# Kernel tuning notes

Measured on AMD Instinct MI355X. Metric: run time of the kernel, lower is better.

Reference implementation:

```python
import jax, jax.numpy as jnp
import numpy as np

N, M, G = 50000, 400000, 128   # nodes, undirected edges, graphs
FN, FE, L, O = 128, 32, 128, 128
MAX_LV = 3


def setup_inputs() -> dict:
    rng = np.random.default_rng(0)
    key = jax.random.key(0)
    ks = jax.random.split(key, 12)
    # random multigraph without self-loops; directed edges interleaved so that
    # edge 2i = (u->v) and edge 2i+1 = (v->u) (reverse edge = e ^ 1)
    u = rng.integers(0, N, size=M)
    v = (u + 1 + rng.integers(0, N - 1, size=M)) % N
    src = np.empty(2 * M, dtype=np.int32)
    dst = np.empty(2 * M, dtype=np.int32)
    src[0::2], src[1::2] = u, v
    dst[0::2], dst[1::2] = v, u
    graph_ids = np.sort(rng.integers(0, G, size=N)).astype(np.int32)

    def lin(k, fan_in, fan_out):
        return jax.random.normal(k, (fan_in, fan_out), jnp.float32) / np.sqrt(fan_in)

    return {
        "node_feat": jax.random.normal(ks[0], (N, FN), jnp.float32),
        "edge_feat": jax.random.normal(ks[1], (2 * M, FE), jnp.float32),
        "w_n2l_W": lin(ks[2], FN, L), "w_n2l_b": jnp.zeros((L,), jnp.float32),
        "w_e2l_W": lin(ks[3], FE, L), "w_e2l_b": jnp.zeros((L,), jnp.float32),
        "conv_W": lin(ks[4], L, L),   "conv_b": jnp.zeros((L,), jnp.float32),
        "out_W": lin(ks[5], L, O),    "out_b": jnp.zeros((O,), jnp.float32),
        "edge_src": jnp.asarray(src),
        "edge_dst": jnp.asarray(dst),
        "graph_ids": jnp.asarray(graph_ids),
        "num_graphs": G,
    }


def _swap_reverse(msgs):
    # message of the reverse directed edge: pairs are interleaved (2i, 2i+1)
    E, D = msgs.shape
    return msgs.reshape(E // 2, 2, D)[:, ::-1, :].reshape(E, D)


def reference(node_feat, edge_feat, w_n2l_W, w_n2l_b, w_e2l_W, w_e2l_b,
              conv_W, conv_b, out_W, out_b, edge_src, edge_dst, graph_ids,
              num_graphs):
    n_nodes = node_feat.shape[0]
    # n2e_sp @ (W_n node_feat): gather source-node linear features onto edges
    input_node_linear = node_feat @ w_n2l_W + w_n2l_b          # [N, L]
    input_message = input_node_linear[edge_src]                # [E, L]
    input_message = input_message + (edge_feat @ w_e2l_W + w_e2l_b)
    cur = jax.nn.relu(input_message)                           # input_potential
    for _ in range(MAX_LV):
        # e2e_sp @ cur: sum of messages into src node, minus reverse edge
        node_agg = jax.ops.segment_sum(cur, edge_dst, num_segments=n_nodes)
        e2epool = node_agg[edge_src] - _swap_reverse(cur)      # [E, L]
        cur = jax.nn.relu(e2epool @ conv_W + conv_b + input_message)
    # e2n_sp @ cur: sum edge messages into destination nodes
    e2npool = jax.ops.segment_sum(cur, edge_dst, num_segments=n_nodes)
    hidden_msg = jax.nn.relu(e2npool)                          # [N, L]
    reluact = jax.nn.relu(hidden_msg @ out_W + out_b)          # [N, O]
    # subg_sp @ reluact: pool nodes per graph
    y = jax.ops.segment_sum(reluact, graph_ids, num_segments=num_graphs)
    return jax.nn.relu(y)                                      # [G, O]
```

## Files before the change

kernel.cpp:

```cpp
#include <hip/hip_runtime.h>
#include <hip/hip_bf16.h>
#include <stdint.h>

typedef __attribute__((ext_vector_type(8))) short short8;
typedef __attribute__((ext_vector_type(4))) float f32x4;

#if defined(__has_builtin)
#if __has_builtin(__builtin_amdgcn_cvt_pk_bf16_f32)
#define HAVE_PK_BF16 1
#endif
#endif

__device__ __forceinline__ float b2f(ushort u) {
  union { uint32_t i; float f; } v; v.i = ((uint32_t)u) << 16; return v.f;
}
__device__ __forceinline__ ushort f2b_sw(float f) {
  union { float f; uint32_t i; } v; v.f = f;
  uint32_t x = v.i;
  uint32_t r = x + 0x7FFFu + ((x >> 16) & 1u);
  return (ushort)(r >> 16);
}
__device__ __forceinline__ uint pk2(float lo, float hi) {
#ifdef HAVE_PK_BF16
  auto r = __builtin_amdgcn_cvt_pk_bf16_f32(lo, hi);
  union { decltype(r) v; uint u; } c; c.v = r; return c.u;
#else
  return (uint)f2b_sw(lo) | ((uint)f2b_sw(hi) << 16);
#endif
}
__device__ __forceinline__ ushort f2b(float f) {
#ifdef HAVE_PK_BF16
  return (ushort)(pk2(f, 0.f) & 0xFFFFu);
#else
  return f2b_sw(f);
#endif
}
__device__ __forceinline__ float lo2f(uint v) { return b2f((ushort)(v & 0xFFFFu)); }
__device__ __forceinline__ float hi2f(uint v) { return b2f((ushort)(v >> 16)); }

__device__ __forceinline__ uint4 pkf8(float4 a, float4 b) {
  uint4 o;
  o.x = pk2(a.x, a.y); o.y = pk2(a.z, a.w);
  o.z = pk2(b.x, b.y); o.w = pk2(b.z, b.w);
  return o;
}
__device__ __forceinline__ uint sub2(uint a, uint b) {
  return pk2(lo2f(a) - lo2f(b), hi2f(a) - hi2f(b));
}
__device__ __forceinline__ uint4 sub8(uint4 a, uint4 b) {
  uint4 o; o.x = sub2(a.x,b.x); o.y = sub2(a.y,b.y); o.z = sub2(a.z,b.z); o.w = sub2(a.w,b.w); return o;
}
__device__ __forceinline__ uint addrelu2(uint a, uint b) {
  return pk2(fmaxf(lo2f(a) + lo2f(b), 0.f), fmaxf(hi2f(a) + hi2f(b), 0.f));
}
__device__ __forceinline__ uint4 addrelu8(uint4 a, uint4 b) {
  uint4 o; o.x = addrelu2(a.x,b.x); o.y = addrelu2(a.y,b.y);
  o.z = addrelu2(a.z,b.z); o.w = addrelu2(a.w,b.w); return o;
}
__device__ __forceinline__ uint relu2(uint v) {
  uint lo = (v & 0x8000u) ? 0u : (v & 0xFFFFu);
  uint hi = (v & 0x80000000u) ? 0u : (v & 0xFFFF0000u);
  return lo | hi;
}
__device__ __forceinline__ uint4 relu8(uint4 v) {
  uint4 o; o.x = relu2(v.x); o.y = relu2(v.y); o.z = relu2(v.z); o.w = relu2(v.w); return o;
}

__global__ void zero_ints(int* __restrict__ p, int n) {
  int i = blockIdx.x * blockDim.x + threadIdx.x;
  if (i < n) p[i] = 0;
}

__global__ void prep_weights(const float* __restrict__ wn, const float* __restrict__ we,
                             const float* __restrict__ cw, const float* __restrict__ ow,
                             const float* __restrict__ cb, const float* __restrict__ be,
                             ushort* __restrict__ wnT, ushort* __restrict__ weT,
                             ushort* __restrict__ cweT, ushort* __restrict__ owT,
                             float* __restrict__ cbe) {
  int i = blockIdx.x * blockDim.x + threadIdx.x;
  if (i < 16384) {
    int n = i >> 7, k = i & 127; wnT[n*128+k] = f2b(wn[k*128+n]);
  } else if (i < 32768) {
    int j = i - 16384; int n = j >> 7, k = j & 127; owT[n*128+k] = f2b(ow[k*128+n]);
  } else if (i < 53248) {
    int j = i - 32768;
    int n = j / 160, k = j % 160;
    cweT[n*160+k] = (k < 128) ? f2b(cw[k*128+n]) : f2b(we[(k-128)*128+n]);
  } else if (i < 57344) {
    int j = i - 53248; int n = j >> 5, k = j & 31; weT[n*32+k] = f2b(we[k*128+n]);
  } else if (i < 57472) {
    int j = i - 57344; cbe[j] = cb[j] + be[j];
  }
}

__global__ void count_dst(const int* __restrict__ dst, int* __restrict__ counts, int E) {
  for (int i = blockIdx.x * blockDim.x + threadIdx.x; i < E; i += gridDim.x * blockDim.x)
    atomicAdd(&counts[dst[i]], 1);
}
__global__ __launch_bounds__(1024) void scan_offsets(
    const int* __restrict__ counts, int* __restrict__ off,
    int* __restrict__ cursor, int N) {
  __shared__ int part[1024];
  int t = threadIdx.x;
  int chunk = (N + 1023) >> 10;
  int lo = t * chunk, hi = min(lo + chunk, N);
  int s = 0;
  for (int i = lo; i < hi; ++i) s += counts[i];
  part[t] = s;
  __syncthreads();
  for (int d = 1; d < 1024; d <<= 1) {
    int v = (t >= d) ? part[t - d] : 0;
    __syncthreads();
    part[t] += v;
    __syncthreads();
  }
  int run = (t > 0) ? part[t - 1] : 0;
  for (int i = lo; i < hi; ++i) {
    off[i] = run; cursor[i] = run; run += counts[i];
  }
  if (t == 1023) off[N] = part[1023];
}
__global__ void fill_csr(const int* __restrict__ dst, int* __restrict__ cursor,
                         int* __restrict__ eids, int E) {
  for (int i = blockIdx.x * blockDim.x + threadIdx.x; i < E; i += gridDim.x * blockDim.x) {
    int p = atomicAdd(&cursor[dst[i]], 1);
    eids[p] = i;
  }
}

__global__ __launch_bounds__(256) void node_linear(
    const float* __restrict__ nf, const ushort* __restrict__ wnT,
    const float* __restrict__ bn, ushort* __restrict__ inl, int N) {
  __shared__ ushort Als[64][136];
  __shared__ ushort Bls[128][136];
  int tid = threadIdx.x;
  int n0 = blockIdx.x * 64;
  {
    int row = tid >> 1, h = tid & 1;
    const uint4* gp = (const uint4*)(wnT + row*128 + h*64);
    uint4* lp = (uint4*)&Bls[row][h*64];
    #pragma unroll
    for (int i = 0; i < 8; ++i) lp[i] = gp[i];
  }
  {
    int r = tid >> 2, q = tid & 3;
    int n = n0 + r;
    uint4* lp = (uint4*)&Als[r][q*32];
    if (n < N) {
      const float4* fp = (const float4*)(nf + (size_t)n*128 + q*32);
      #pragma unroll
      for (int i = 0; i < 4; ++i) lp[i] = pkf8(fp[2*i], fp[2*i+1]);
    } else {
      uint4 z = {0,0,0,0};
      #pragma unroll
      for (int i = 0; i < 4; ++i) lp[i] = z;
    }
  }
  __syncthreads();
  int l = tid & 63, w = tid >> 6, quad = l >> 4, mr = l & 15;
  f32x4 acc[8];
  #pragma unroll
  for (int nt = 0; nt < 8; ++nt) acc[nt] = (f32x4){0.f,0.f,0.f,0.f};
  #pragma unroll
  for (int kk = 0; kk < 4; ++kk) {
    short8 a = *(const short8*)&Als[w*16 + mr][kk*32 + quad*8];
    #pragma unroll
    for (int nt = 0; nt < 8; ++nt) {
      short8 b = *(const short8*)&Bls[nt*16 + mr][kk*32 + quad*8];
      acc[nt] = __builtin_amdgcn_mfma_f32_16x16x32_bf16(a, b, acc[nt], 0, 0, 0);
    }
  }
  #pragma unroll
  for (int nt = 0; nt < 8; ++nt) {
    int col = nt*16 + mr;
    float bias = bn[col];
    #pragma unroll
    for (int rg = 0; rg < 4; ++rg) {
      int n = n0 + w*16 + quad*4 + rg;
      if (n < N) inl[(size_t)n*128 + col] = f2b(acc[nt][rg] + bias);
    }
  }
}

__global__ __launch_bounds__(256) void edge_init(
    const float* __restrict__ ef, const ushort* __restrict__ weT,
    const float* __restrict__ be, const int* __restrict__ esrc,
    const ushort* __restrict__ inl, ushort* __restrict__ cur,
    ushort* __restrict__ efb, int E) {
  __shared__ ushort Als[64][40];
  __shared__ ushort Cls[64][136];
  int tid = threadIdx.x;
  int e0 = blockIdx.x * 64;
  int l = tid & 63, w = tid >> 6, quad = l >> 4, mr = l & 15;
  int r = tid >> 2, q = tid & 3;

  short8 bfrag[2];
  #pragma unroll
  for (int nt = 0; nt < 2; ++nt)
    bfrag[nt] = *(const short8*)(weT + (size_t)(w*32 + nt*16 + mr)*32 + quad*8);

  {
    const float4* fp = (const float4*)(ef + (size_t)(e0 + r)*32 + q*8);
    uint4 pk = pkf8(fp[0], fp[1]);
    *(uint4*)&Als[r][q*8] = pk;
    if (efb) *(uint4*)(efb + (size_t)(e0 + r)*32 + q*8) = pk;
  }
  __syncthreads();

  int col0 = w*32 + mr, col1 = w*32 + 16 + mr;
  float bias0 = be[col0], bias1 = be[col1];
  #pragma unroll
  for (int m = 0; m < 4; ++m) {
    short8 a = *(const short8*)&Als[m*16 + mr][quad*8];
    f32x4 zero = (f32x4){0.f,0.f,0.f,0.f};
    f32x4 acc0 = __builtin_amdgcn_mfma_f32_16x16x32_bf16(a, bfrag[0], zero, 0, 0, 0);
    f32x4 acc1 = __builtin_amdgcn_mfma_f32_16x16x32_bf16(a, bfrag[1], zero, 0, 0, 0);
    #pragma unroll
    for (int rg = 0; rg < 4; ++rg) {
      int row = m*16 + quad*4 + rg;
      Cls[row][col0] = f2b(acc0[rg] + bias0);
      Cls[row][col1] = f2b(acc1[rg] + bias1);
    }
  }
  __syncthreads();

  {
    int e = e0 + r;
    int s = esrc[e];
    const uint4* cl = (const uint4*)&Cls[r][q*32];
    const uint4* ip = (const uint4*)(inl + (size_t)s*128 + q*32);
    uint4* op = (uint4*)(cur + (size_t)e*128 + q*32);
    #pragma unroll
    for (int i = 0; i < 4; ++i) op[i] = addrelu8(cl[i], ip[i]);
  }
}

__global__ __launch_bounds__(256) void segsum(
    const ushort* __restrict__ cur, const int* __restrict__ off,
    const int* __restrict__ eids, ushort* __restrict__ nagg, int N) {
  int w = threadIdx.x >> 6, l = threadIdx.x & 63;
  int n = blockIdx.x * 4 + w;
  if (n >= N) return;
  int i = off[n], end = off[n + 1];
  float s0 = 0.f, s1 = 0.f;
  for (; i + 8 <= end; i += 8) {
    int e[8]; uint v[8];
    #pragma unroll
    for (int j = 0; j < 8; ++j) e[j] = eids[i + j];
    #pragma unroll
    for (int j = 0; j < 8; ++j) v[j] = *(const uint*)(cur + (size_t)e[j]*128 + 2*l);
    #pragma unroll
    for (int j = 0; j < 8; ++j) { s0 += lo2f(v[j]); s1 += hi2f(v[j]); }
  }
  for (; i < end; ++i) {
    int ea = eids[i];
    uint va = *(const uint*)(cur + (size_t)ea*128 + 2*l);
    s0 += lo2f(va); s1 += hi2f(va);
  }
  *(uint*)(nagg + (size_t)n*128 + 2*l) = pk2(s0, s1);
}

__global__ __launch_bounds__(256) void conv_step(
    ushort* __restrict__ cur, const ushort* __restrict__ nagg,
    const ushort* __restrict__ inl, const ushort* __restrict__ efb,
    const float* __restrict__ ef, const ushort* __restrict__ cweT,
    const float* __restrict__ cbe, const int* __restrict__ esrc, int E) {
  __shared__ ushort Als[64][168];
  int tid = threadIdx.x;
  int e0 = blockIdx.x * 64;
  int l = tid & 63, w = tid >> 6, quad = l >> 4, mr = l & 15;
  int r = tid >> 2, q = tid & 3;

  short8 bfrag[2][5];
  #pragma unroll
  for (int nt = 0; nt < 2; ++nt) {
    const ushort* bp = cweT + (size_t)(w*32 + nt*16 + mr) * 160;
    #pragma unroll
    for (int kk = 0; kk < 5; ++kk)
      bfrag[nt][kk] = *(const short8*)(bp + kk*32 + quad*8);
  }

  {
    int e = e0 + r;
    int s = esrc[e];
    const uint4* cp = (const uint4*)(cur + (size_t)(e ^ 1)*128 + q*32);
    const uint4* np = (const uint4*)(nagg + (size_t)s*128 + q*32);
    uint4* lp = (uint4*)&Als[r][q*32];
    #pragma unroll
    for (int i = 0; i < 4; ++i) lp[i] = sub8(np[i], cp[i]);
    if (efb) {
      *(uint4*)&Als[r][128 + q*8] = *(const uint4*)(efb + (size_t)e*32 + q*8);
    } else {
      const float4* fp = (const float4*)(ef + (size_t)e*32 + q*8);
      *(uint4*)&Als[r][128 + q*8] = pkf8(fp[0], fp[1]);
    }
  }
  __syncthreads();

  int col0 = w*32 + mr, col1 = w*32 + 16 + mr;
  float bias0 = cbe[col0], bias1 = cbe[col1];
  f32x4 acc0[4], acc1[4];
  #pragma unroll
  for (int m = 0; m < 4; ++m) {
    acc0[m] = (f32x4){0.f,0.f,0.f,0.f};
    acc1[m] = (f32x4){0.f,0.f,0.f,0.f};
    #pragma unroll
    for (int kk = 0; kk < 5; ++kk) {
      short8 a = *(const short8*)&Als[m*16 + mr][kk*32 + quad*8];
      acc0[m] = __builtin_amdgcn_mfma_f32_16x16x32_bf16(a, bfrag[0][kk], acc0[m], 0, 0, 0);
      acc1[m] = __builtin_amdgcn_mfma_f32_16x16x32_bf16(a, bfrag[1][kk], acc1[m], 0, 0, 0);
    }
  }
  __syncthreads();

  #pragma unroll
  for (int m = 0; m < 4; ++m) {
    #pragma unroll
    for (int rg = 0; rg < 4; ++rg) {
      int row = m*16 + quad*4 + rg;
      Als[row][col0] = f2b(acc0[m][rg] + bias0);
      Als[row][col1] = f2b(acc1[m][rg] + bias1);
    }
  }
  __syncthreads();

  {
    int e = e0 + r;
    int s = esrc[e];
    const uint4* cl = (const uint4*)&Als[r][q*32];
    const uint4* ip = (const uint4*)(inl + (size_t)s*128 + q*32);
    uint4* op = (uint4*)(cur + (size_t)e*128 + q*32);
    #pragma unroll
    for (int i = 0; i < 4; ++i) op[i] = addrelu8(cl[i], ip[i]);
  }
}

__global__ __launch_bounds__(256) void out_linear(
    const ushort* __restrict__ nagg, const ushort* __restrict__ owT,
    const float* __restrict__ ob, ushort* __restrict__ ract, int N) {
  __shared__ ushort Als[64][136];
  __shared__ ushort Bls[128][136];
  int tid = threadIdx.x;
  int n0 = blockIdx.x * 64;
  {
    int row = tid >> 1, h = tid & 1;
    const uint4* gp = (const uint4*)(owT + row*128 + h*64);
    uint4* lp = (uint4*)&Bls[row][h*64];
    #pragma unroll
    for (int i = 0; i < 8; ++i) lp[i] = gp[i];
  }
  {
    int r = tid >> 2, q = tid & 3;
    int n = n0 + r;
    uint4* lp = (uint4*)&Als[r][q*32];
    if (n < N) {
      const uint4* gp = (const uint4*)(nagg + (size_t)n*128 + q*32);
      #pragma unroll
      for (int i = 0; i < 4; ++i) lp[i] = relu8(gp[i]);
    } else {
      uint4 z = {0,0,0,0};
      #pragma unroll
      for (int i = 0; i < 4; ++i) lp[i] = z;
    }
  }
  __syncthreads();
  int l = tid & 63, w = tid >> 6, quad = l >> 4, mr = l & 15;
  f32x4 acc[8];
  #pragma unroll
  for (int nt = 0; nt < 8; ++nt) acc[nt] = (f32x4){0.f,0.f,0.f,0.f};
  #pragma unroll
  for (int kk = 0; kk < 4; ++kk) {
    short8 a = *(const short8*)&Als[w*16 + mr][kk*32 + quad*8];
    #pragma unroll
    for (int nt = 0; nt < 8; ++nt) {
      short8 b = *(const short8*)&Bls[nt*16 + mr][kk*32 + quad*8];
      acc[nt] = __builtin_amdgcn_mfma_f32_16x16x32_bf16(a, b, acc[nt], 0, 0, 0);
    }
  }
  #pragma unroll
  for (int nt = 0; nt < 8; ++nt) {
    int col = nt*16 + mr;
    float bias = ob[col];
    #pragma unroll
    for (int rg = 0; rg < 4; ++rg) {
      int n = n0 + w*16 + quad*4 + rg;
      if (n < N) ract[(size_t)n*128 + col] = f2b(fmaxf(acc[nt][rg] + bias, 0.f));
    }
  }
}

__global__ void graph_offsets(const int* __restrict__ gids, int* __restrict__ goff,
                              int N, int G) {
  int i = blockIdx.x * blockDim.x + threadIdx.x;
  if (i > N) return;
  int pg = (i == 0) ? -1 : gids[i - 1];
  int cg = (i == N) ? G : gids[i];
  for (int g = pg + 1; g <= cg; ++g) goff[g] = i;
}

__global__ __launch_bounds__(256) void graph_pool(
    const ushort* __restrict__ ract, const int* __restrict__ goff,
    float* __restrict__ out, int G) {
  __shared__ float red0[256];
  __shared__ float red1[256];
  int g = blockIdx.x;
  int t = threadIdx.x;
  int c2 = t & 63, rp = t >> 6;
  int beg = goff[g], end = goff[g + 1];
  float s0 = 0.f, s1 = 0.f;
  for (int n = beg + rp; n < end; n += 4) {
    uint v = *(const uint*)(ract + (size_t)n*128 + 2*c2);
    s0 += lo2f(v); s1 += hi2f(v);
  }
  red0[t] = s0; red1[t] = s1;
  __syncthreads();
  if (rp == 0) {
    float v0 = red0[c2] + red0[c2 + 64] + red0[c2 + 128] + red0[c2 + 192];
    float v1 = red1[c2] + red1[c2 + 64] + red1[c2 + 128] + red1[c2 + 192];
    float2 o; o.x = fmaxf(v0, 0.f); o.y = fmaxf(v1, 0.f);
    *(float2*)(out + (size_t)g*128 + 2*c2) = o;
  }
}

extern "C" void kernel_launch(void* const* d_in, const int* in_sizes, int n_in,
                              void* d_out, int out_size, void* d_ws, size_t ws_size,
                              hipStream_t stream) {
  const float* node_feat = (const float*)d_in[0];
  const float* edge_feat = (const float*)d_in[1];
  const float* wn = (const float*)d_in[2];
  const float* bn = (const float*)d_in[3];
  const float* we = (const float*)d_in[4];
  const float* be = (const float*)d_in[5];
  const float* cw = (const float*)d_in[6];
  const float* cb = (const float*)d_in[7];
  const float* ow = (const float*)d_in[8];
  const float* ob = (const float*)d_in[9];
  const int* esrc = (const int*)d_in[10];
  const int* edst = (const int*)d_in[11];
  const int* gids = (const int*)d_in[12];
  int N = in_sizes[0] / 128;
  int E = in_sizes[10];
  int G = out_size / 128;
  float* out = (float*)d_out;

  char* p = (char*)d_ws;
  auto alloc = [&](size_t bytes) {
    char* r = p;
    p += (bytes + 255) & ~(size_t)255;
    return r;
  };
  ushort* cur     = (ushort*)alloc((size_t)E * 128 * 2);
  ushort* inl     = (ushort*)alloc((size_t)N * 128 * 2);
  ushort* nagg    = (ushort*)alloc((size_t)N * 128 * 2);
  int*    eids    = (int*)   alloc((size_t)E * 4);
  int*    counts  = (int*)   alloc((size_t)N * 4);
  int*    off     = (int*)   alloc((size_t)(N + 1) * 4);
  int*    cursor  = (int*)   alloc((size_t)N * 4);
  int*    goff    = (int*)   alloc((size_t)(G + 1) * 4);
  ushort* wnT     = (ushort*)alloc(128 * 128 * 2);
  ushort* weT     = (ushort*)alloc(128 * 32 * 2);
  ushort* cweT    = (ushort*)alloc(128 * 160 * 2);
  ushort* owT     = (ushort*)alloc(128 * 128 * 2);
  float*  cbe     = (float*) alloc(128 * 4);
  ushort* efb     = (ushort*)alloc((size_t)E * 32 * 2);
  if ((size_t)(p - (char*)d_ws) > ws_size) efb = nullptr;
  ushort* ract    = inl;
  (void)n_in;

  zero_ints<<<(N + 255) / 256, 256, 0, stream>>>(counts, N);
  prep_weights<<<225, 256, 0, stream>>>(wn, we, cw, ow, cb, be, wnT, weT, cweT, owT, cbe);
  count_dst<<<1024, 256, 0, stream>>>(edst, counts, E);
  scan_offsets<<<1, 1024, 0, stream>>>(counts, off, cursor, N);
  fill_csr<<<1024, 256, 0, stream>>>(edst, cursor, eids, E);

  node_linear<<<(N + 63) / 64, 256, 0, stream>>>(node_feat, wnT, bn, inl, N);
  edge_init<<<E / 64, 256, 0, stream>>>(edge_feat, weT, be, esrc, inl, cur, efb, E);

  for (int it = 0; it < 3; ++it) {
    segsum<<<(N + 3) / 4, 256, 0, stream>>>(cur, off, eids, nagg, N);
    conv_step<<<E / 64, 256, 0, stream>>>(cur, nagg, inl, efb, edge_feat, cweT, cbe, esrc, E);
  }
  segsum<<<(N + 3) / 4, 256, 0, stream>>>(cur, off, eids, nagg, N);
  out_linear<<<(N + 63) / 64, 256, 0, stream>>>(nagg, owT, ob, ract, N);
  graph_offsets<<<(N + 256) / 256, 256, 0, stream>>>(gids, goff, N, G);
  graph_pool<<<G, 256, 0, stream>>>(ract, goff, out, G);
}
```

Baseline: 1.188 ms.

## Interleave node aggregate and input-linear rows, widen segsum gathers across half-waves

```diff
diff --git a/kernel.cpp b/kernel.cpp
--- a/kernel.cpp
+++ b/kernel.cpp
@@ -130,7 +130,7 @@
 
 __global__ __launch_bounds__(256) void node_linear(
     const float* __restrict__ nf, const ushort* __restrict__ wnT,
-    const float* __restrict__ bn, ushort* __restrict__ inl, int N) {
+    const float* __restrict__ bn, ushort* __restrict__ ni, int N) {
   __shared__ ushort Als[64][136];
   __shared__ ushort Bls[128][136];
   int tid = threadIdx.x;
@@ -177,7 +177,7 @@
     #pragma unroll
     for (int rg = 0; rg < 4; ++rg) {
       int n = n0 + w*16 + quad*4 + rg;
-      if (n < N) inl[(size_t)n*128 + col] = f2b(acc[nt][rg] + bias);
+      if (n < N) ni[(size_t)n*256 + 128 + col] = f2b(acc[nt][rg] + bias);
     }
   }
 }
@@ -185,7 +185,7 @@
 __global__ __launch_bounds__(256) void edge_init(
     const float* __restrict__ ef, const ushort* __restrict__ weT,
     const float* __restrict__ be, const int* __restrict__ esrc,
-    const ushort* __restrict__ inl, ushort* __restrict__ cur,
+    const ushort* __restrict__ ni, ushort* __restrict__ cur,
     ushort* __restrict__ efb, int E) {
   __shared__ ushort Als[64][40];
   __shared__ ushort Cls[64][136];
@@ -199,11 +199,19 @@
   for (int nt = 0; nt < 2; ++nt)
     bfrag[nt] = *(const short8*)(weT + (size_t)(w*32 + nt*16 + mr)*32 + quad*8);
 
-  {
-    const float4* fp = (const float4*)(ef + (size_t)(e0 + r)*32 + q*8);
+  int e = e0 + r;
+  int s = esrc[e];
+  {
+    const float4* fp = (const float4*)(ef + (size_t)e*32 + q*8);
     uint4 pk = pkf8(fp[0], fp[1]);
     *(uint4*)&Als[r][q*8] = pk;
-    if (efb) *(uint4*)(efb + (size_t)(e0 + r)*32 + q*8) = pk;
+    if (efb) *(uint4*)(efb + (size_t)e*32 + q*8) = pk;
+  }
+  uint4 irow[4];
+  {
+    const uint4* ip = (const uint4*)(ni + (size_t)s*256 + 128 + q*32);
+    #pragma unroll
+    for (int i = 0; i < 4; ++i) irow[i] = ip[i];
   }
   __syncthreads();
 
@@ -225,46 +233,60 @@
   __syncthreads();
 
   {
-    int e = e0 + r;
-    int s = esrc[e];
     const uint4* cl = (const uint4*)&Cls[r][q*32];
-    const uint4* ip = (const uint4*)(inl + (size_t)s*128 + q*32);
     uint4* op = (uint4*)(cur + (size_t)e*128 + q*32);
     #pragma unroll
-    for (int i = 0; i < 4; ++i) op[i] = addrelu8(cl[i], ip[i]);
+    for (int i = 0; i < 4; ++i) op[i] = addrelu8(cl[i], irow[i]);
   }
 }
 
 __global__ __launch_bounds__(256) void segsum(
     const ushort* __restrict__ cur, const int* __restrict__ off,
-    const int* __restrict__ eids, ushort* __restrict__ nagg, int N) {
+    const int* __restrict__ eids, ushort* __restrict__ ni, int N) {
   int w = threadIdx.x >> 6, l = threadIdx.x & 63;
   int n = blockIdx.x * 4 + w;
   if (n >= N) return;
-  int i = off[n], end = off[n + 1];
-  float s0 = 0.f, s1 = 0.f;
-  for (; i + 8 <= end; i += 8) {
-    int e[8]; uint v[8];
-    #pragma unroll
-    for (int j = 0; j < 8; ++j) e[j] = eids[i + j];
-    #pragma unroll
-    for (int j = 0; j < 8; ++j) v[j] = *(const uint*)(cur + (size_t)e[j]*128 + 2*l);
-    #pragma unroll
-    for (int j = 0; j < 8; ++j) { s0 += lo2f(v[j]); s1 += hi2f(v[j]); }
-  }
-  for (; i < end; ++i) {
-    int ea = eids[i];
-    uint va = *(const uint*)(cur + (size_t)ea*128 + 2*l);
-    s0 += lo2f(va); s1 += hi2f(va);
-  }
-  *(uint*)(nagg + (size_t)n*128 + 2*l) = pk2(s0, s1);
+  int c8 = l & 31;
+  int half = l >> 5;
+  int beg = off[n], end = off[n + 1];
+  float s0 = 0.f, s1 = 0.f, s2 = 0.f, s3 = 0.f;
+  int i = beg;
+  for (; i + 16 <= end; i += 16) {
+    uint2 v[8];
+    #pragma unroll
+    for (int j = 0; j < 8; ++j) {
+      int e = eids[i + 2*j + half];
+      v[j] = *(const uint2*)(cur + (size_t)e*128 + c8*4);
+    }
+    #pragma unroll
+    for (int j = 0; j < 8; ++j) {
+      s0 += lo2f(v[j].x); s1 += hi2f(v[j].x);
+      s2 += lo2f(v[j].y); s3 += hi2f(v[j].y);
+    }
+  }
+  for (; i + 2 <= end; i += 2) {
+    int e = eids[i + half];
+    uint2 v = *(const uint2*)(cur + (size_t)e*128 + c8*4);
+    s0 += lo2f(v.x); s1 += hi2f(v.x); s2 += lo2f(v.y); s3 += hi2f(v.y);
+  }
+  if (i < end && half == 0) {
+    int e = eids[i];
+    uint2 v = *(const uint2*)(cur + (size_t)e*128 + c8*4);
+    s0 += lo2f(v.x); s1 += hi2f(v.x); s2 += lo2f(v.y); s3 += hi2f(v.y);
+  }
+  s0 += __shfl_xor(s0, 32); s1 += __shfl_xor(s1, 32);
+  s2 += __shfl_xor(s2, 32); s3 += __shfl_xor(s3, 32);
+  if (half == 0) {
+    uint2 o; o.x = pk2(s0, s1); o.y = pk2(s2, s3);
+    *(uint2*)(ni + (size_t)n*256 + c8*4) = o;
+  }
 }
 
 __global__ __launch_bounds__(256) void conv_step(
-    ushort* __restrict__ cur, const ushort* __restrict__ nagg,
-    const ushort* __restrict__ inl, const ushort* __restrict__ efb,
-    const float* __restrict__ ef, const ushort* __restrict__ cweT,
-    const float* __restrict__ cbe, const int* __restrict__ esrc, int E) {
+    ushort* __restrict__ cur, const ushort* __restrict__ ni,
+    const ushort* __restrict__ efb, const float* __restrict__ ef,
+    const ushort* __restrict__ cweT, const float* __restrict__ cbe,
+    const int* __restrict__ esrc, int E) {
   __shared__ ushort Als[64][168];
   int tid = threadIdx.x;
   int e0 = blockIdx.x * 64;
@@ -280,11 +302,11 @@
       bfrag[nt][kk] = *(const short8*)(bp + kk*32 + quad*8);
   }
 
-  {
-    int e = e0 + r;
-    int s = esrc[e];
+  int e = e0 + r;
+  int s = esrc[e];
+  {
     const uint4* cp = (const uint4*)(cur + (size_t)(e ^ 1)*128 + q*32);
-    const uint4* np = (const uint4*)(nagg + (size_t)s*128 + q*32);
+    const uint4* np = (const uint4*)(ni + (size_t)s*256 + q*32);
     uint4* lp = (uint4*)&Als[r][q*32];
     #pragma unroll
     for (int i = 0; i < 4; ++i) lp[i] = sub8(np[i], cp[i]);
@@ -295,6 +317,12 @@
       *(uint4*)&Als[r][128 + q*8] = pkf8(fp[0], fp[1]);
     }
   }
+  uint4 irow[4];
+  {
+    const uint4* ip = (const uint4*)(ni + (size_t)s*256 + 128 + q*32);
+    #pragma unroll
+    for (int i = 0; i < 4; ++i) irow[i] = ip[i];
+  }
   __syncthreads();
 
   int col0 = w*32 + mr, col1 = w*32 + 16 + mr;
@@ -325,18 +353,15 @@
   __syncthreads();
 
   {
-    int e = e0 + r;
-    int s = esrc[e];
     const uint4* cl = (const uint4*)&Als[r][q*32];
-    const uint4* ip = (const uint4*)(inl + (size_t)s*128 + q*32);
     uint4* op = (uint4*)(cur + (size_t)e*128 + q*32);
     #pragma unroll
-    for (int i = 0; i < 4; ++i) op[i] = addrelu8(cl[i], ip[i]);
+    for (int i = 0; i < 4; ++i) op[i] = addrelu8(cl[i], irow[i]);
   }
 }
 
 __global__ __launch_bounds__(256) void out_linear(
-    const ushort* __restrict__ nagg, const ushort* __restrict__ owT,
+    const ushort* __restrict__ ni, const ushort* __restrict__ owT,
     const float* __restrict__ ob, ushort* __restrict__ ract, int N) {
   __shared__ ushort Als[64][136];
   __shared__ ushort Bls[128][136];
@@ -354,7 +379,7 @@
     int n = n0 + r;
     uint4* lp = (uint4*)&Als[r][q*32];
     if (n < N) {
-      const uint4* gp = (const uint4*)(nagg + (size_t)n*128 + q*32);
+      const uint4* gp = (const uint4*)(ni + (size_t)n*256 + q*32);
       #pragma unroll
       for (int i = 0; i < 4; ++i) lp[i] = relu8(gp[i]);
     } else {
@@ -450,8 +475,7 @@
     return r;
   };
   ushort* cur     = (ushort*)alloc((size_t)E * 128 * 2);
-  ushort* inl     = (ushort*)alloc((size_t)N * 128 * 2);
-  ushort* nagg    = (ushort*)alloc((size_t)N * 128 * 2);
+  ushort* ni      = (ushort*)alloc((size_t)N * 256 * 2);
   int*    eids    = (int*)   alloc((size_t)E * 4);
   int*    counts  = (int*)   alloc((size_t)N * 4);
   int*    off     = (int*)   alloc((size_t)(N + 1) * 4);
@@ -464,7 +488,7 @@
   float*  cbe     = (float*) alloc(128 * 4);
   ushort* efb     = (ushort*)alloc((size_t)E * 32 * 2);
   if ((size_t)(p - (char*)d_ws) > ws_size) efb = nullptr;
-  ushort* ract    = inl;
+  ushort* ract    = cur;
   (void)n_in;
 
   zero_ints<<<(N + 255) / 256, 256, 0, stream>>>(counts, N);
@@ -473,15 +497,15 @@
   scan_offsets<<<1, 1024, 0, stream>>>(counts, off, cursor, N);
   fill_csr<<<1024, 256, 0, stream>>>(edst, cursor, eids, E);
 
-  node_linear<<<(N + 63) / 64, 256, 0, stream>>>(node_feat, wnT, bn, inl, N);
-  edge_init<<<E / 64, 256, 0, stream>>>(edge_feat, weT, be, esrc, inl, cur, efb, E);
+  node_linear<<<(N + 63) / 64, 256, 0, stream>>>(node_feat, wnT, bn, ni, N);
+  edge_init<<<E / 64, 256, 0, stream>>>(edge_feat, weT, be, esrc, ni, cur, efb, E);
 
   for (int it = 0; it < 3; ++it) {
-    segsum<<<(N + 3) / 4, 256, 0, stream>>>(cur, off, eids, nagg, N);
-    conv_step<<<E / 64, 256, 0, stream>>>(cur, nagg, inl, efb, edge_feat, cweT, cbe, esrc, E);
-  }
-  segsum<<<(N + 3) / 4, 256, 0, stream>>>(cur, off, eids, nagg, N);
-  out_linear<<<(N + 63) / 64, 256, 0, stream>>>(nagg, owT, ob, ract, N);
+    segsum<<<(N + 3) / 4, 256, 0, stream>>>(cur, off, eids, ni, N);
+    conv_step<<<E / 64, 256, 0, stream>>>(cur, ni, efb, edge_feat, cweT, cbe, esrc, E);
+  }
+  segsum<<<(N + 3) / 4, 256, 0, stream>>>(cur, off, eids, ni, N);
+  out_linear<<<(N + 63) / 64, 256, 0, stream>>>(ni, owT, ob, ract, N);
   graph_offsets<<<(N + 256) / 256, 256, 0, stream>>>(gids, goff, N, G);
   graph_pool<<<G, 256, 0, stream>>>(ract, goff, out, G);
 }
```

Measured after the change: 1.153 ms. -3.0%, faster.
